# Optimization experiments

Hardware: AMD Instinct MI355X
Metric: run time of the kernel (lower is better)

The kernel has to match this reference:

```python
import jax, jax.numpy as jnp
import numpy as np

N_REGIONS = 17
N_CH = 7
ROWS, COLS = 82, 67
N_CELLS = 3000
BATCH = 2048


def setup_inputs() -> dict:
    key = jax.random.key(0)
    k1, k2 = jax.random.split(key)
    x = jax.random.normal(k1, (BATCH, N_REGIONS * N_CH), dtype=jnp.float32)
    # distinct linear cell indices -> unique (row, col) pairs
    cell_lin = jnp.arange(N_CELLS, dtype=jnp.int64)
    region_ids = jax.random.randint(k2, (N_CELLS,), 0, N_REGIONS, dtype=jnp.int64)
    return {"x": x, "cell_lin": cell_lin, "region_ids": region_ids}


def reference(x, cell_lin, region_ids):
    B = x.shape[0]
    reshaped = x.reshape(B, N_REGIONS, N_CH)          # (B, 17, 7)
    rows = cell_lin // COLS                           # (M,)
    cols = cell_lin % COLS                            # (M,)
    updates = reshaped[:, region_ids, :]              # (B, M, 7) gather per cell
    out = jnp.zeros((B, ROWS, COLS, N_CH), dtype=x.dtype)
    out = out.at[rows, cols].set(updates.transpose(1, 0, 2).reshape(N_CELLS, B, N_CH).transpose(0, 1, 2), mode="drop") if False else out.at[:, rows, cols, :].set(updates)
    return out
```

## Files before the change

kernel.cpp:

```cpp
#include <hip/hip_runtime.h>

#define N_REGIONS 17
#define N_CH 7
#define ROWS_ 82
#define COLS_ 67
#define N_MAP (ROWS_ * COLS_)
#define EPB (N_MAP * N_CH)
#define PAIR (2 * EPB)
#define XROW (N_REGIONS * N_CH)

typedef float f32x4 __attribute__((ext_vector_type(4)));


__global__ void init_table_k(short* __restrict__ t) {
    int i = blockIdx.x * blockDim.x + threadIdx.x;
    if (i < PAIR) t[i] = -1;
}

__global__ void scatter_table_k(const int* __restrict__ cell_lin,
                                const int* __restrict__ region_ids,
                                int n, short* __restrict__ t) {
    int i = blockIdx.x * blockDim.x + threadIdx.x;
    if (i >= n) return;
    int c = cell_lin[i];
    int r = region_ids[i];
    if (c < 0 || c >= N_MAP) return;
#pragma unroll
    for (int lb = 0; lb < 2; ++lb) {
        int dst = lb * EPB + c * N_CH;
        short src = (short)(lb * XROW + r * N_CH);
#pragma unroll
        for (int ch = 0; ch < N_CH; ++ch) t[dst + ch] = (short)(src + ch);
    }
}

__global__ __launch_bounds__(256) void fill2_k(const float* __restrict__ x,
                                               const short* __restrict__ t,
                                               float* __restrict__ out,
                                               unsigned total4) {
    unsigned stride = gridDim.x * blockDim.x;
    for (unsigned i = blockIdx.x * blockDim.x + threadIdx.x; i < total4; i += stride) {
        unsigned e0 = i * 4u;
        unsigned p = e0 / PAIR;
        unsigned off = e0 - p * PAIR;
        short4 s = *reinterpret_cast<const short4*>(t + off);
        const float* xb = x + p * (2 * XROW);
        f32x4 v;
        v.x = (s.x >= 0) ? xb[s.x] : 0.0f;
        v.y = (s.y >= 0) ? xb[s.y] : 0.0f;
        v.z = (s.z >= 0) ? xb[s.z] : 0.0f;
        v.w = (s.w >= 0) ? xb[s.w] : 0.0f;
        __builtin_nontemporal_store(v, reinterpret_cast<f32x4*>(out + e0));
    }
}

extern "C" void kernel_launch(void* const* d_in, const int* in_sizes, int n_in,
                              void* d_out, int out_size, void* d_ws, size_t ws_size,
                              hipStream_t stream) {
    const float* x        = (const float*)d_in[0];
    const int* cell_lin   = (const int*)d_in[1];
    const int* region_ids = (const int*)d_in[2];
    float* out = (float*)d_out;
    short* table = (short*)d_ws;
    int n_cells = in_sizes[1];

    init_table_k<<<(PAIR + 255) / 256, 256, 0, stream>>>(table);
    scatter_table_k<<<(n_cells + 255) / 256, 256, 0, stream>>>(cell_lin, region_ids, n_cells, table);

    unsigned total4 = (unsigned)out_size / 4u;
    fill2_k<<<2048, 256, 0, stream>>>(x, table, out, total4);
}
```

Baseline: 72.96 us.

## Stage per-pair input row in LDS and assign one block per half-pair

The fill kernel moves from a grid-stride loop with per-element division to a fixed mapping where each block handles half of one batch pair. The pair's 238 input floats go into shared memory, and the lookups read from LDS instead of global memory. This removes the integer divide and the scattered global gathers. In exchange it hardcodes the batch size through a launch of 2048 blocks, and the half split constant assumes a specific output size.

```diff
diff --git a/kernel.cpp b/kernel.cpp
--- a/kernel.cpp
+++ b/kernel.cpp
@@ -7,7 +7,10 @@
 #define N_MAP (ROWS_ * COLS_)
 #define EPB (N_MAP * N_CH)
 #define PAIR (2 * EPB)
+#define PAIR4 (PAIR / 4)
+#define HALF4 9615
 #define XROW (N_REGIONS * N_CH)
+#define XPAIR (2 * XROW)
 
 typedef float f32x4 __attribute__((ext_vector_type(4)));
 
@@ -34,23 +37,28 @@
     }
 }
 
-__global__ __launch_bounds__(256) void fill2_k(const float* __restrict__ x,
+__global__ __launch_bounds__(256) void fill3_k(const float* __restrict__ x,
                                                const short* __restrict__ t,
-                                               float* __restrict__ out,
-                                               unsigned total4) {
-    unsigned stride = gridDim.x * blockDim.x;
-    for (unsigned i = blockIdx.x * blockDim.x + threadIdx.x; i < total4; i += stride) {
+                                               float* __restrict__ out) {
+    __shared__ float xs[XPAIR];
+    unsigned pair = blockIdx.x >> 1;
+    unsigned half = blockIdx.x & 1;
+    unsigned tid = threadIdx.x;
+    if (tid < XPAIR) xs[tid] = x[pair * XPAIR + tid];
+    __syncthreads();
+
+    unsigned start = half ? HALF4 : 0;
+    unsigned end   = half ? PAIR4 : HALF4;
+    float* outp = out + (size_t)pair * PAIR;
+    for (unsigned i = start + tid; i < end; i += 256) {
         unsigned e0 = i * 4u;
-        unsigned p = e0 / PAIR;
-        unsigned off = e0 - p * PAIR;
-        short4 s = *reinterpret_cast<const short4*>(t + off);
-        const float* xb = x + p * (2 * XROW);
+        short4 s = *reinterpret_cast<const short4*>(t + e0);
         f32x4 v;
-        v.x = (s.x >= 0) ? xb[s.x] : 0.0f;
-        v.y = (s.y >= 0) ? xb[s.y] : 0.0f;
-        v.z = (s.z >= 0) ? xb[s.z] : 0.0f;
-        v.w = (s.w >= 0) ? xb[s.w] : 0.0f;
-        __builtin_nontemporal_store(v, reinterpret_cast<f32x4*>(out + e0));
+        v.x = (s.x >= 0) ? xs[s.x] : 0.0f;
+        v.y = (s.y >= 0) ? xs[s.y] : 0.0f;
+        v.z = (s.z >= 0) ? xs[s.z] : 0.0f;
+        v.w = (s.w >= 0) ? xs[s.w] : 0.0f;
+        __builtin_nontemporal_store(v, reinterpret_cast<f32x4*>(outp + e0));
     }
 }
 
@@ -67,6 +75,5 @@
     init_table_k<<<(PAIR + 255) / 256, 256, 0, stream>>>(table);
     scatter_table_k<<<(n_cells + 255) / 256, 256, 0, stream>>>(cell_lin, region_ids, n_cells, table);
 
-    unsigned total4 = (unsigned)out_size / 4u;
-    fill2_k<<<2048, 256, 0, stream>>>(x, table, out, total4);
+    fill3_k<<<2048, 256, 0, stream>>>(x, table, out);
 }
```

Result: slower. 96.41 us (+32.1%).

## Copy x into padded workspace and gather with two vector loads per quad

Applied to the files above, without the earlier changes.

The table init kernel now also copies x into the workspace, with a guard gap so that out-of-range vector reads stay in bounds, and empty slots use a negative sentinel. The fill kernel replaces four scalar gathers per output quad with two 16-byte loads anchored at the first and last indices and picks lanes by contiguity. It skips the loads when a whole wavefront sees only empty slots. This trades scattered scalar loads for wider loads at the cost of an extra copy of x, and it hardcodes the batch size and map dimensions.

```diff
diff --git a/kernel.cpp b/kernel.cpp
--- a/kernel.cpp
+++ b/kernel.cpp
@@ -1,40 +1,42 @@
 #include <hip/hip_runtime.h>
 
-#define N_REGIONS 17
 #define N_CH 7
-#define ROWS_ 82
-#define COLS_ 67
-#define N_MAP (ROWS_ * COLS_)
-#define EPB (N_MAP * N_CH)
-#define PAIR (2 * EPB)
-#define XROW (N_REGIONS * N_CH)
+#define N_MAP 5494
+#define EPB 38458u
+#define PAIR 76916u
+#define XROW 119
+#define XPAIR 238
+#define XTOT (2048 * XROW)
+#define SENT (-8)
 
 typedef float f32x4 __attribute__((ext_vector_type(4)));
 
+#define XCOPY_BYTE_OFF (153856 + 64)
 
-__global__ void init_table_k(short* __restrict__ t) {
+__global__ void prep_k(const float* __restrict__ x, short* __restrict__ t,
+                       float* __restrict__ xc) {
     int i = blockIdx.x * blockDim.x + threadIdx.x;
-    if (i < PAIR) t[i] = -1;
+    if (i < (int)PAIR) t[i] = SENT;
+    if (i < XTOT) xc[i] = x[i];
 }
 
-__global__ void scatter_table_k(const int* __restrict__ cell_lin,
-                                const int* __restrict__ region_ids,
+__global__ void scatter_table_k(const int* __restrict__ cl,
+                                const int* __restrict__ rid,
                                 int n, short* __restrict__ t) {
     int i = blockIdx.x * blockDim.x + threadIdx.x;
     if (i >= n) return;
-    int c = cell_lin[i];
-    int r = region_ids[i];
+    int c = cl[i], r = rid[i];
     if (c < 0 || c >= N_MAP) return;
 #pragma unroll
     for (int lb = 0; lb < 2; ++lb) {
-        int dst = lb * EPB + c * N_CH;
+        int dst = lb * (int)EPB + c * N_CH;
         short src = (short)(lb * XROW + r * N_CH);
 #pragma unroll
         for (int ch = 0; ch < N_CH; ++ch) t[dst + ch] = (short)(src + ch);
     }
 }
 
-__global__ __launch_bounds__(256) void fill2_k(const float* __restrict__ x,
+__global__ __launch_bounds__(256) void fill6_k(const float* __restrict__ xc,
                                                const short* __restrict__ t,
                                                float* __restrict__ out,
                                                unsigned total4) {
@@ -44,12 +46,16 @@
         unsigned p = e0 / PAIR;
         unsigned off = e0 - p * PAIR;
         short4 s = *reinterpret_cast<const short4*>(t + off);
-        const float* xb = x + p * (2 * XROW);
-        f32x4 v;
-        v.x = (s.x >= 0) ? xb[s.x] : 0.0f;
-        v.y = (s.y >= 0) ? xb[s.y] : 0.0f;
-        v.z = (s.z >= 0) ? xb[s.z] : 0.0f;
-        v.w = (s.w >= 0) ? xb[s.w] : 0.0f;
+        f32x4 v = {0.f, 0.f, 0.f, 0.f};
+        if (__any((s.x >= 0) || (s.w >= 0))) {
+            const float* xb = xc + p * XPAIR;
+            f32x4 A = *reinterpret_cast<const f32x4*>(xb + (int)s.x);
+            f32x4 B = *reinterpret_cast<const f32x4*>(xb + (int)s.w - 3);
+            v.x = (s.x >= 0) ? A.x : 0.f;
+            v.y = (s.y >= 0) ? ((s.y == s.x + 1) ? A.y : B.y) : 0.f;
+            v.z = (s.z >= 0) ? ((s.z == s.x + 2) ? A.z : B.z) : 0.f;
+            v.w = (s.w >= 0) ? B.w : 0.f;
+        }
         __builtin_nontemporal_store(v, reinterpret_cast<f32x4*>(out + e0));
     }
 }
@@ -62,11 +68,12 @@
     const int* region_ids = (const int*)d_in[2];
     float* out = (float*)d_out;
     short* table = (short*)d_ws;
+    float* xcopy = (float*)((char*)d_ws + XCOPY_BYTE_OFF);
     int n_cells = in_sizes[1];
 
-    init_table_k<<<(PAIR + 255) / 256, 256, 0, stream>>>(table);
+    prep_k<<<(XTOT + 255) / 256, 256, 0, stream>>>(x, table, xcopy);
     scatter_table_k<<<(n_cells + 255) / 256, 256, 0, stream>>>(cell_lin, region_ids, n_cells, table);
 
     unsigned total4 = (unsigned)out_size / 4u;
-    fill2_k<<<2048, 256, 0, stream>>>(x, table, out, total4);
+    fill6_k<<<2048, 256, 0, stream>>>(xcopy, table, out, total4);
 }
```

New measurement: 66.88 us. -8.3%, faster.
